# Kernel optimization log

Hardware: AMD Instinct MI355X
Metric: run time of the kernel (lower is better)

The kernel has to match this reference:

```python
import jax, jax.numpy as jnp
import numpy as np

N, F_IN, F_OUT = 8192, 512, 64
LEAKY_ALPHA = 0.2
NEG_MASK = -9e15


def setup_inputs() -> dict:
    key = jax.random.key(0)
    k1, k2, k3, k4 = jax.random.split(key, 4)
    x = jax.random.normal(k1, (N, F_IN), dtype=jnp.float32)
    adj = jax.random.randint(k2, (N, N), 0, 2, dtype=jnp.int32)
    # xavier-normal-ish scale for params
    W = jax.random.normal(k3, (F_IN, F_OUT), dtype=jnp.float32) * np.sqrt(2.0 / (F_IN + F_OUT)).astype(np.float32)
    a = jax.random.normal(k4, (2 * F_OUT, 1), dtype=jnp.float32) * np.sqrt(2.0 / (2 * F_OUT + 1)).astype(np.float32)
    return {"x": x, "adj": adj, "W": W, "a": a}


def reference(x, adj, W, a):
    # eval mode: dropout is identity
    Wh = x @ W                                   # [N, F_out]
    wh_i = Wh @ a[:F_OUT, :]                     # [N, 1]
    wh_j = Wh @ a[F_OUT:, :]                     # [N, 1]
    e = wh_i + wh_j.T                            # [N, N] broadcast add
    e = jnp.where(e >= 0, e, LEAKY_ALPHA * e)    # leaky_relu
    e = jnp.where(adj > 0, e, NEG_MASK)
    attn = jax.nn.softmax(e, axis=1)             # row-wise softmax
    h = attn @ Wh                                # [N, F_out]
    # ELU activation
    return jax.nn.elu(h)
```

## Files before the change

kernel.cpp:

```cpp
#include <hip/hip_runtime.h>

#define NN 8192
#define FIN 512
#define FO 64

typedef short bf16x8 __attribute__((ext_vector_type(8)));
typedef float f32x4 __attribute__((ext_vector_type(4)));

union AFrag { bf16x8 v; __bf16 b[8]; };

__global__ __launch_bounds__(512) void wt_kernel(const float* __restrict__ W, __bf16* __restrict__ WT) {
    __shared__ float tile[64][65];
    const int k0 = blockIdx.x * 64;
    #pragma unroll
    for (int r = 0; r < 8; ++r) {
        const int kl = r * 8 + (threadIdx.x >> 6);
        const int f  = threadIdx.x & 63;
        tile[kl][f] = W[(size_t)(k0 + kl) * FO + f];
    }
    __syncthreads();
    const int f   = threadIdx.x >> 3;
    const int kk8 = (threadIdx.x & 7) * 8;
    unsigned u[4];
    #pragma unroll
    for (int h = 0; h < 4; ++h) {
        union { __bf16 b; unsigned short us; } lo, hi;
        lo.b = (__bf16)tile[kk8 + 2*h][f];
        hi.b = (__bf16)tile[kk8 + 2*h + 1][f];
        u[h] = (unsigned)lo.us | ((unsigned)hi.us << 16);
    }
    *(uint4*)(WT + (size_t)f * FIN + k0 + kk8) = make_uint4(u[0], u[1], u[2], u[3]);
}

__global__ __launch_bounds__(128) void wh_kernel(
    const float* __restrict__ x, const __bf16* __restrict__ WT,
    const float* __restrict__ a, uint4* __restrict__ whs,
    float* __restrict__ s_out, float* __restrict__ t_out)
{
    __shared__ float whlds[2][16][FO + 1];
    const int w  = threadIdx.x >> 6;
    const int l  = threadIdx.x & 63;
    const int lr = l & 15, lg = l >> 4;
    const int rb = (blockIdx.x * 2 + w) * 16;

    f32x4 acc[4] = {};
    const float* xr = x + (size_t)(rb + lr) * FIN;
    const __bf16* wbase[4];
    #pragma unroll
    for (int ft = 0; ft < 4; ++ft) wbase[ft] = WT + (ft*16 + lr) * FIN;

    float4 nxa = *(const float4*)(xr + lg*4);
    float4 nxb = *(const float4*)(xr + lg*4 + 16);
    for (int ks = 0; ks < 16; ++ks) {
        const int k0 = ks*32 + lg*4;
        const float4 xa = nxa, xb = nxb;
        const int kn = (ks < 15 ? ks + 1 : 15)*32 + lg*4;
        nxa = *(const float4*)(xr + kn);
        nxb = *(const float4*)(xr + kn + 16);
        AFrag af;
        af.b[0]=(__bf16)xa.x; af.b[1]=(__bf16)xa.y; af.b[2]=(__bf16)xa.z; af.b[3]=(__bf16)xa.w;
        af.b[4]=(__bf16)xb.x; af.b[5]=(__bf16)xb.y; af.b[6]=(__bf16)xb.z; af.b[7]=(__bf16)xb.w;
        #pragma unroll
        for (int ft = 0; ft < 4; ++ft) {
            union { bf16x8 v; uint2 q[2]; } bf;
            bf.q[0] = *(const uint2*)(wbase[ft] + k0);
            bf.q[1] = *(const uint2*)(wbase[ft] + k0 + 16);
            acc[ft] = __builtin_amdgcn_mfma_f32_16x16x32_bf16(af.v, bf.v, acc[ft], 0, 0, 0);
        }
    }

    #pragma unroll
    for (int ft = 0; ft < 4; ++ft)
        #pragma unroll
        for (int q = 0; q < 4; ++q)
            whlds[w][lg*4+q][ft*16+lr] = acc[ft][q];

    float sp[4] = {0,0,0,0}, tp[4] = {0,0,0,0};
    #pragma unroll
    for (int ft = 0; ft < 4; ++ft) {
        const float a1 = a[ft*16 + lr];
        const float a2 = a[FO + ft*16 + lr];
        #pragma unroll
        for (int q = 0; q < 4; ++q) { sp[q] += acc[ft][q]*a1; tp[q] += acc[ft][q]*a2; }
    }
    #pragma unroll
    for (int d = 1; d < 16; d <<= 1) {
        #pragma unroll
        for (int q = 0; q < 4; ++q) { sp[q] += __shfl_xor(sp[q], d); tp[q] += __shfl_xor(tp[q], d); }
    }
    if (lr == 0) {
        *(float4*)(s_out + rb + lg*4) = make_float4(sp[0], sp[1], sp[2], sp[3]);
        *(float4*)(t_out + rb + lg*4) = make_float4(tp[0], tp[1], tp[2], tp[3]);
    }

    __syncthreads();

    const int jb = blockIdx.x;
    #pragma unroll
    for (int q = 0; q < 2; ++q) {
        const int ft = w*2 + q;
        const int f  = ft*16 + lr;
        unsigned u[4];
        #pragma unroll
        for (int h = 0; h < 4; ++h) {
            const int c0 = ((h & 2) ? 16 : 0) + lg*4 + (h & 1)*2;
            union { __bf16 b; unsigned short us; } lo, hi;
            lo.b = (__bf16)whlds[c0 >> 4][c0 & 15][f];
            hi.b = (__bf16)whlds[(c0+1) >> 4][(c0+1) & 15][f];
            u[h] = (unsigned)lo.us | ((unsigned)hi.us << 16);
        }
        whs[(jb*4 + ft)*64 + l] = make_uint4(u[0], u[1], u[2], u[3]);
    }
}

__global__ __launch_bounds__(1024, 4) void gat_kernel(
    const int* __restrict__ adj, const uint4* __restrict__ whs,
    const float* __restrict__ s_in, const float* __restrict__ t_in,
    float* __restrict__ out)
{
    __shared__ __align__(16) unsigned char plds[2][16384];
    __shared__ float dnl[16];
    const int w  = threadIdx.x >> 6;
    const int l  = threadIdx.x & 63;
    const int lr = l & 15, lg = l >> 4;
    const int rg = blockIdx.x;
    const int row = rg * 16 + w;
    const float sv = s_in[row];
    const int* adjr = adj + (size_t)row * NN;
    const bf16x8* wv = (const bf16x8*)whs;

    const int lane0 = w + ((l & 3) << 4);
    const int halfb = ((l >> 2) & 1) << 3;
    const int jbA = l >> 3, jbB = 8 + (l >> 3);
    const int wa0 = ((((jbA << 6) + lane0) << 4) + halfb) ^ ((jbA & 7) << 4) ^ ((l & 3) << 5);
    const int wa1 = ((((jbB << 6) + lane0) << 4) + halfb) ^ ((jbB & 7) << 4) ^ ((l & 3) << 5);
    const int ra  = ((((w << 6) + l) << 4)) ^ ((w & 7) << 4) ^ ((lg & 3) << 5);

    f32x4 acc[4] = {};
    float dn = 0.f;

    int4   A0 = *(const int4*)(adjr + l*4);
    int4   A1 = *(const int4*)(adjr + 256 + l*4);
    float4 T0 = *(const float4*)(t_in + l*4);
    float4 T1 = *(const float4*)(t_in + 256 + l*4);
    bf16x8 bv[2][4];
    #pragma unroll
    for (int ft = 0; ft < 4; ++ft) bv[0][ft] = wv[(w*4 + ft)*64 + l];

    #pragma unroll 2
    for (int it = 0; it < 16; ++it) {
        const int   av[8] = {A0.x, A0.y, A0.z, A0.w, A1.x, A1.y, A1.z, A1.w};
        const float tv[8] = {T0.x, T0.y, T0.z, T0.w, T1.x, T1.y, T1.z, T1.w};

        const int cn = (it == 15) ? 0 : (it + 1) * 512;
        A0 = *(const int4*)(adjr + cn + l*4);
        A1 = *(const int4*)(adjr + cn + 256 + l*4);
        T0 = *(const float4*)(t_in + cn + l*4);
        T1 = *(const float4*)(t_in + cn + 256 + l*4);
        const int jn = ((it == 15) ? 0 : ((it + 1) * 16 + w)) * 4;
        #pragma unroll
        for (int ft = 0; ft < 4; ++ft) bv[(it + 1) & 1][ft] = wv[(jn + ft)*64 + l];

        unsigned pk[4];
        #pragma unroll
        for (int i = 0; i < 4; ++i) {
            float e0 = sv + tv[2*i];     e0 = fmaxf(e0, 0.2f * e0);
            float e1 = sv + tv[2*i + 1]; e1 = fmaxf(e1, 0.2f * e1);
            const float p0 = av[2*i]     ? __expf(e0) : 0.f;
            const float p1 = av[2*i + 1] ? __expf(e1) : 0.f;
            dn += p0 + p1;
            union { __bf16 b; unsigned short u; } c0, c1;
            c0.b = (__bf16)p0; c1.b = (__bf16)p1;
            pk[i] = (unsigned)c0.u | ((unsigned)c1.u << 16);
        }
        *(uint2*)(plds[it & 1] + wa0) = make_uint2(pk[0], pk[1]);
        *(uint2*)(plds[it & 1] + wa1) = make_uint2(pk[2], pk[3]);

        asm volatile("s_waitcnt lgkmcnt(0)\n\ts_barrier" ::: "memory");

        AFrag af;
        af.v = *(const bf16x8*)(plds[it & 1] + ra);
        #pragma unroll
        for (int ft = 0; ft < 4; ++ft)
            acc[ft] = __builtin_amdgcn_mfma_f32_16x16x32_bf16(af.v, bv[it & 1][ft], acc[ft], 0, 0, 0);
    }

    #pragma unroll
    for (int d = 1; d < 64; d <<= 1) dn += __shfl_xor(dn, d);
    if (l == 0) dnl[w] = dn;

    float* red = (float*)plds;
    #pragma unroll
    for (int h = 8; h >= 1; h >>= 1) {
        __syncthreads();
        if (w >= h && w < 2*h) {
            #pragma unroll
            for (int ft = 0; ft < 4; ++ft)
                #pragma unroll
                for (int q = 0; q < 4; ++q)
                    red[(((w - h) * 16) + ft*4 + q)*64 + l] = acc[ft][q];
        }
        __syncthreads();
        if (w < h) {
            #pragma unroll
            for (int ft = 0; ft < 4; ++ft)
                #pragma unroll
                for (int q = 0; q < 4; ++q)
                    acc[ft][q] += red[((w * 16) + ft*4 + q)*64 + l];
        }
    }

    if (w == 0) {
        #pragma unroll
        for (int ft = 0; ft < 4; ++ft) {
            #pragma unroll
            for (int q = 0; q < 4; ++q) {
                const int m = lg*4 + q;
                const float h2 = acc[ft][q] / dnl[m];
                out[(size_t)(rg*16 + m) * FO + ft*16 + lr] =
                    (h2 > 0.f) ? h2 : (__expf(h2) - 1.f);
            }
        }
    }
}

extern "C" void kernel_launch(void* const* d_in, const int* in_sizes, int n_in,
                              void* d_out, int out_size, void* d_ws, size_t ws_size,
                              hipStream_t stream) {
    const float* x   = (const float*)d_in[0];
    const int*   adj = (const int*)d_in[1];
    const float* W   = (const float*)d_in[2];
    const float* a   = (const float*)d_in[3];
    float* out = (float*)d_out;

    char* ws = (char*)d_ws;
    uint4*  whs = (uint4*)ws;
    __bf16* WT  = (__bf16*)(ws + (1u << 20));
    float*  s   = (float*)(ws + (1u << 20) + (1u << 16));
    float*  t   = (float*)(ws + (1u << 20) + (1u << 16) + 32768);

    wt_kernel<<<8, 512, 0, stream>>>(W, WT);
    wh_kernel<<<256, 128, 0, stream>>>(x, WT, a, whs, s, t);
    gat_kernel<<<512, 1024, 0, stream>>>(adj, whs, s, t, out);
}
```

Measured before the change: 93.63 us.

## Compress adjacency to bitmask and process 32 rows per block

```diff
diff --git a/kernel.cpp b/kernel.cpp
--- a/kernel.cpp
+++ b/kernel.cpp
@@ -113,112 +113,129 @@
     }
 }
 
-__global__ __launch_bounds__(1024, 4) void gat_kernel(
-    const int* __restrict__ adj, const uint4* __restrict__ whs,
+__global__ __launch_bounds__(256) void mask_kernel(
+    const int* __restrict__ adj, unsigned* __restrict__ mask)
+{
+    const int l   = threadIdx.x & 63;
+    const int wid = (blockIdx.x * 256 + threadIdx.x) >> 6;
+    #pragma unroll 4
+    for (int g = wid; g < NN * 128; g += 4096) {
+        const int v = adj[(size_t)g * 64 + l];
+        const unsigned long long b = __ballot(v != 0);
+        if (l == 0)
+            *(uint2*)(mask + (size_t)g * 2) = make_uint2((unsigned)b, (unsigned)(b >> 32));
+    }
+}
+
+__global__ __launch_bounds__(1024, 4) void gat3_kernel(
+    const unsigned* __restrict__ mask, const uint4* __restrict__ whs,
     const float* __restrict__ s_in, const float* __restrict__ t_in,
     float* __restrict__ out)
 {
-    __shared__ __align__(16) unsigned char plds[2][16384];
-    __shared__ float dnl[16];
+    __shared__ float red[8][2048];
+    __shared__ float dnl[16][32];
+    __shared__ float dns[32];
     const int w  = threadIdx.x >> 6;
     const int l  = threadIdx.x & 63;
     const int lr = l & 15, lg = l >> 4;
     const int rg = blockIdx.x;
-    const int row = rg * 16 + w;
-    const float sv = s_in[row];
-    const int* adjr = adj + (size_t)row * NN;
+    const int r0 = rg * 32;
+    const float sA = s_in[r0 + lr];
+    const float sB = s_in[r0 + 16 + lr];
+    const unsigned* mrowA = mask + (size_t)(r0 + lr) * 256;
+    const unsigned* mrowB = mask + (size_t)(r0 + 16 + lr) * 256;
+    const int sh0 = lg * 4;
     const bf16x8* wv = (const bf16x8*)whs;
 
-    const int lane0 = w + ((l & 3) << 4);
-    const int halfb = ((l >> 2) & 1) << 3;
-    const int jbA = l >> 3, jbB = 8 + (l >> 3);
-    const int wa0 = ((((jbA << 6) + lane0) << 4) + halfb) ^ ((jbA & 7) << 4) ^ ((l & 3) << 5);
-    const int wa1 = ((((jbB << 6) + lane0) << 4) + halfb) ^ ((jbB & 7) << 4) ^ ((l & 3) << 5);
-    const int ra  = ((((w << 6) + l) << 4)) ^ ((w & 7) << 4) ^ ((lg & 3) << 5);
-
-    f32x4 acc[4] = {};
-    float dn = 0.f;
-
-    int4   A0 = *(const int4*)(adjr + l*4);
-    int4   A1 = *(const int4*)(adjr + 256 + l*4);
-    float4 T0 = *(const float4*)(t_in + l*4);
-    float4 T1 = *(const float4*)(t_in + 256 + l*4);
-    bf16x8 bv[2][4];
-    #pragma unroll
-    for (int ft = 0; ft < 4; ++ft) bv[0][ft] = wv[(w*4 + ft)*64 + l];
-
-    #pragma unroll 2
+    f32x4 acc[2][4] = {};
+    float dnA = 0.f, dnB = 0.f;
+
+    unsigned mA = mrowA[w*16], mB = mrowB[w*16];
+    float4 t0 = *(const float4*)(t_in + w*512 + sh0);
+    float4 t1 = *(const float4*)(t_in + w*512 + 16 + sh0);
+
     for (int it = 0; it < 16; ++it) {
-        const int   av[8] = {A0.x, A0.y, A0.z, A0.w, A1.x, A1.y, A1.z, A1.w};
-        const float tv[8] = {T0.x, T0.y, T0.z, T0.w, T1.x, T1.y, T1.z, T1.w};
-
-        const int cn = (it == 15) ? 0 : (it + 1) * 512;
-        A0 = *(const int4*)(adjr + cn + l*4);
-        A1 = *(const int4*)(adjr + cn + 256 + l*4);
-        T0 = *(const float4*)(t_in + cn + l*4);
-        T1 = *(const float4*)(t_in + cn + 256 + l*4);
-        const int jn = ((it == 15) ? 0 : ((it + 1) * 16 + w)) * 4;
-        #pragma unroll
-        for (int ft = 0; ft < 4; ++ft) bv[(it + 1) & 1][ft] = wv[(jn + ft)*64 + l];
-
-        unsigned pk[4];
-        #pragma unroll
-        for (int i = 0; i < 4; ++i) {
-            float e0 = sv + tv[2*i];     e0 = fmaxf(e0, 0.2f * e0);
-            float e1 = sv + tv[2*i + 1]; e1 = fmaxf(e1, 0.2f * e1);
-            const float p0 = av[2*i]     ? __expf(e0) : 0.f;
-            const float p1 = av[2*i + 1] ? __expf(e1) : 0.f;
-            dn += p0 + p1;
-            union { __bf16 b; unsigned short u; } c0, c1;
-            c0.b = (__bf16)p0; c1.b = (__bf16)p1;
-            pk[i] = (unsigned)c0.u | ((unsigned)c1.u << 16);
-        }
-        *(uint2*)(plds[it & 1] + wa0) = make_uint2(pk[0], pk[1]);
-        *(uint2*)(plds[it & 1] + wa1) = make_uint2(pk[2], pk[3]);
-
-        asm volatile("s_waitcnt lgkmcnt(0)\n\ts_barrier" ::: "memory");
-
-        AFrag af;
-        af.v = *(const bf16x8*)(plds[it & 1] + ra);
-        #pragma unroll
-        for (int ft = 0; ft < 4; ++ft)
-            acc[ft] = __builtin_amdgcn_mfma_f32_16x16x32_bf16(af.v, bv[it & 1][ft], acc[ft], 0, 0, 0);
-    }
-
-    #pragma unroll
-    for (int d = 1; d < 64; d <<= 1) dn += __shfl_xor(dn, d);
-    if (l == 0) dnl[w] = dn;
-
-    float* red = (float*)plds;
-    #pragma unroll
+        const int jb = w*16 + it;
+        bf16x8 bv0 = wv[(jb*4 + 0)*64 + l];
+        bf16x8 bv1 = wv[(jb*4 + 1)*64 + l];
+        bf16x8 bv2 = wv[(jb*4 + 2)*64 + l];
+        bf16x8 bv3 = wv[(jb*4 + 3)*64 + l];
+        const int jn = w*16 + (it + 1 < 16 ? it + 1 : 15);
+        const unsigned nmA = mrowA[jn], nmB = mrowB[jn];
+        const float4 nt0 = *(const float4*)(t_in + jn*32 + sh0);
+        const float4 nt1 = *(const float4*)(t_in + jn*32 + 16 + sh0);
+
+        const float tv[8] = {t0.x, t0.y, t0.z, t0.w, t1.x, t1.y, t1.z, t1.w};
+        AFrag afA, afB;
+        #pragma unroll
+        for (int e = 0; e < 8; ++e) {
+            const int bit = (e < 4) ? (sh0 + e) : (12 + sh0 + e);
+            float eA = sA + tv[e]; eA = fmaxf(eA, 0.2f * eA);
+            float eB = sB + tv[e]; eB = fmaxf(eB, 0.2f * eB);
+            const float pA = ((mA >> bit) & 1u) ? __expf(eA) : 0.f;
+            const float pB = ((mB >> bit) & 1u) ? __expf(eB) : 0.f;
+            dnA += pA; dnB += pB;
+            afA.b[e] = (__bf16)pA;
+            afB.b[e] = (__bf16)pB;
+        }
+        acc[0][0] = __builtin_amdgcn_mfma_f32_16x16x32_bf16(afA.v, bv0, acc[0][0], 0, 0, 0);
+        acc[0][1] = __builtin_amdgcn_mfma_f32_16x16x32_bf16(afA.v, bv1, acc[0][1], 0, 0, 0);
+        acc[0][2] = __builtin_amdgcn_mfma_f32_16x16x32_bf16(afA.v, bv2, acc[0][2], 0, 0, 0);
+        acc[0][3] = __builtin_amdgcn_mfma_f32_16x16x32_bf16(afA.v, bv3, acc[0][3], 0, 0, 0);
+        acc[1][0] = __builtin_amdgcn_mfma_f32_16x16x32_bf16(afB.v, bv0, acc[1][0], 0, 0, 0);
+        acc[1][1] = __builtin_amdgcn_mfma_f32_16x16x32_bf16(afB.v, bv1, acc[1][1], 0, 0, 0);
+        acc[1][2] = __builtin_amdgcn_mfma_f32_16x16x32_bf16(afB.v, bv2, acc[1][2], 0, 0, 0);
+        acc[1][3] = __builtin_amdgcn_mfma_f32_16x16x32_bf16(afB.v, bv3, acc[1][3], 0, 0, 0);
+
+        mA = nmA; mB = nmB; t0 = nt0; t1 = nt1;
+    }
+
+    dnA += __shfl_xor(dnA, 16); dnA += __shfl_xor(dnA, 32);
+    dnB += __shfl_xor(dnB, 16); dnB += __shfl_xor(dnB, 32);
+    if (l < 16) { dnl[w][l] = dnA; dnl[w][16 + l] = dnB; }
+    __syncthreads();
+    if (threadIdx.x < 32) {
+        float s = 0.f;
+        #pragma unroll
+        for (int ww = 0; ww < 16; ++ww) s += dnl[ww][threadIdx.x];
+        dns[threadIdx.x] = s;
+    }
+
     for (int h = 8; h >= 1; h >>= 1) {
-        __syncthreads();
         if (w >= h && w < 2*h) {
             #pragma unroll
-            for (int ft = 0; ft < 4; ++ft)
+            for (int g = 0; g < 2; ++g)
                 #pragma unroll
-                for (int q = 0; q < 4; ++q)
-                    red[(((w - h) * 16) + ft*4 + q)*64 + l] = acc[ft][q];
+                for (int ft = 0; ft < 4; ++ft)
+                    #pragma unroll
+                    for (int q = 0; q < 4; ++q)
+                        red[w - h][((g*16 + lg*4 + q)*FO) + ft*16 + lr] = acc[g][ft][q];
         }
         __syncthreads();
         if (w < h) {
             #pragma unroll
-            for (int ft = 0; ft < 4; ++ft)
+            for (int g = 0; g < 2; ++g)
                 #pragma unroll
-                for (int q = 0; q < 4; ++q)
-                    acc[ft][q] += red[((w * 16) + ft*4 + q)*64 + l];
-        }
+                for (int ft = 0; ft < 4; ++ft)
+                    #pragma unroll
+                    for (int q = 0; q < 4; ++q)
+                        acc[g][ft][q] += red[w][((g*16 + lg*4 + q)*FO) + ft*16 + lr];
+        }
+        __syncthreads();
     }
 
     if (w == 0) {
         #pragma unroll
-        for (int ft = 0; ft < 4; ++ft) {
+        for (int g = 0; g < 2; ++g) {
             #pragma unroll
-            for (int q = 0; q < 4; ++q) {
-                const int m = lg*4 + q;
-                const float h2 = acc[ft][q] / dnl[m];
-                out[(size_t)(rg*16 + m) * FO + ft*16 + lr] =
-                    (h2 > 0.f) ? h2 : (__expf(h2) - 1.f);
+            for (int ft = 0; ft < 4; ++ft) {
+                #pragma unroll
+                for (int q = 0; q < 4; ++q) {
+                    const int m = g*16 + lg*4 + q;
+                    const float h2 = acc[g][ft][q] / dns[m];
+                    out[(size_t)(r0 + m) * FO + ft*16 + lr] =
+                        (h2 > 0.f) ? h2 : (__expf(h2) - 1.f);
+                }
             }
         }
     }
@@ -234,12 +251,14 @@
     float* out = (float*)d_out;
 
     char* ws = (char*)d_ws;
-    uint4*  whs = (uint4*)ws;
-    __bf16* WT  = (__bf16*)(ws + (1u << 20));
-    float*  s   = (float*)(ws + (1u << 20) + (1u << 16));
-    float*  t   = (float*)(ws + (1u << 20) + (1u << 16) + 32768);
-
-    wt_kernel<<<8, 512, 0, stream>>>(W, WT);
-    wh_kernel<<<256, 128, 0, stream>>>(x, WT, a, whs, s, t);
-    gat_kernel<<<512, 1024, 0, stream>>>(adj, whs, s, t, out);
-}
+    uint4*    whs  = (uint4*)ws;
+    __bf16*   WT   = (__bf16*)(ws + (1u << 20));
+    float*    s    = (float*)(ws + (1u << 20) + (1u << 16));
+    float*    t    = (float*)(ws + (1u << 20) + (1u << 16) + 32768);
+    unsigned* mask = (unsigned*)(ws + (2u << 20));
+
+    wt_kernel  <<<8,    512, 0, stream>>>(W, WT);
+    wh_kernel  <<<256,  128, 0, stream>>>(x, WT, a, whs, s, t);
+    mask_kernel<<<1024, 256, 0, stream>>>(adj, mask);
+    gat3_kernel<<<256, 1024, 0, stream>>>(mask, whs, s, t, out);
+}
```

New measurement: 190.9 us. 104% more time.
